# Kernel optimization log

Measured on AMD Instinct MI355X. Metric: run time of the kernel, lower is better.

The kernel has to match this reference:

```python
import jax, jax.numpy as jnp
import numpy as np

H = 8          # heads
D = 64         # head_dimension
EMB = 512      # embedding_dimension
B, S, XL, KK = 4, 1024, 1024, 32


def setup_inputs() -> dict:
    key = jax.random.key(0)
    ks = jax.random.split(key, 14)
    HD = H * D
    wsc = EMB ** -0.5
    return {
        "x": jax.random.normal(ks[0], (B, S, EMB), jnp.float32),
        "rel_pos": jax.random.normal(ks[1], (H, S, XL + S), jnp.float32) * 0.02,
        "xl_memory": jax.random.normal(ks[2], (B, XL, 2, HD), jnp.float32),
        "knn_retrieved": jax.random.normal(ks[3], (B, S, KK, 2, HD), jnp.float32),
        "Wq": jax.random.normal(ks[4], (HD, EMB), jnp.float32) * wsc,
        "bq": jnp.zeros((HD,), jnp.float32),
        "Wk": jax.random.normal(ks[5], (HD, EMB), jnp.float32) * wsc,
        "bk": jnp.zeros((HD,), jnp.float32),
        "Wv": jax.random.normal(ks[6], (HD, EMB), jnp.float32) * wsc,
        "bv": jnp.zeros((HD,), jnp.float32),
        "Wo": jax.random.normal(ks[7], (EMB, HD), jnp.float32) * (HD ** -0.5),
        "bo": jnp.zeros((EMB,), jnp.float32),
        "gate": jax.random.normal(ks[8], (H, 1, 1), jnp.float32),
    }


def _split_heads(t):
    # [b, s, h*d] -> [b, h, s, d]
    b, s, _ = t.shape
    return t.reshape(b, s, H, D).transpose(0, 2, 1, 3)


def reference(x, rel_pos, xl_memory, knn_retrieved,
              Wq, bq, Wk, bk, Wv, bv, Wo, bo, gate):
    scale = D ** -0.5
    b, s, _ = x.shape
    xl_len = xl_memory.shape[1]

    q = _split_heads(x @ Wq.T + bq)   # [b,h,s,d]
    k = _split_heads(x @ Wk.T + bk)
    v = _split_heads(x @ Wv.T + bv)

    # XL memory concat (keys/values stacked along dim -2 of xl_memory)
    k_mem = _split_heads(xl_memory[..., 0, :])
    v_mem = _split_heads(xl_memory[..., 1, :])
    k = jnp.concatenate((k_mem, k), axis=2)  # [b,h,j,d], j = xl+s
    v = jnp.concatenate((v_mem, v), axis=2)

    # local causal XL attention; note: rel_pos added BEFORE scaling (as in source)
    qk = jnp.einsum('bhid,bhjd->bhij', q, k)
    i, j = qk.shape[-2:]
    qk = (qk + rel_pos[..., -i:, -j:]) * scale
    mask = jnp.triu(jnp.ones((i, j), dtype=bool), j - i + 1)
    attn = jax.nn.softmax(jnp.where(mask, -jnp.inf, qk), axis=-1)
    qkv = jnp.einsum('bhij,bhjd->bhid', attn, v)

    # kNN external-memory attention over retrieved kv pairs
    kk = knn_retrieved.shape[2]
    k_ext = knn_retrieved[..., 0, :].reshape(b, s, kk, H, D).transpose(0, 3, 1, 2, 4)  # [b,h,s,k,d]
    v_ext = knn_retrieved[..., 1, :].reshape(b, s, kk, H, D).transpose(0, 3, 1, 2, 4)
    qk_ext = jnp.einsum('bhsd,bhskd->bhsk', q, k_ext) * scale
    attn_ext = jax.nn.softmax(qk_ext, axis=-1)
    qkv_ext = jnp.einsum('bhsk,bhskd->bhsd', attn_ext, v_ext)

    g = jax.nn.sigmoid(gate)                # [h,1,1] broadcasts over [b,h,s,d]
    merged = qkv * g + qkv_ext * (1.0 - g)

    out = merged.transpose(0, 2, 1, 3).reshape(b, s, H * D) @ Wo.T + bo

    # current kv memory: flatten heads, stack (k,v), drop the xl prefix
    key_flat = k.transpose(0, 2, 1, 3).reshape(b, j, H * D)
    val_flat = v.transpose(0, 2, 1, 3).reshape(b, j, H * D)
    current_kv_memory = jnp.stack((key_flat, val_flat), axis=-2)[:, xl_len:]

    return out, current_kv_memory
```

## Files before the change

kernel.cpp:

```cpp
#include <hip/hip_runtime.h>
#include <stdint.h>

#define H_ 8
#define D_ 64
#define EMBD 512
#define HD_ 512
#define B_ 4
#define S_ 1024
#define XL_ 1024
#define J_ 2048
#define KK_ 32
#define OUT1 (B_*S_*EMBD)

typedef __bf16 bf16x8 __attribute__((ext_vector_type(8)));
typedef float f32x4 __attribute__((ext_vector_type(4)));

__device__ __forceinline__ uint32_t pack2bf(float a, float b) {
    uint32_t ua = __builtin_bit_cast(uint32_t, a);
    uint32_t ub = __builtin_bit_cast(uint32_t, b);
    ua = (ua + 0x7FFFu + ((ua >> 16) & 1u)) >> 16;
    ub = (ub + 0x7FFFu + ((ub >> 16) & 1u)) >> 16;
    return ua | (ub << 16);
}

#define GPAD 72

__device__ __forceinline__ void gemm_tile_body(
    const float* __restrict__ A, const float* __restrict__ W,
    const float* __restrict__ bias, float* __restrict__ out, int mode,
    uint16_t* a_l, uint16_t* w_l, int m0, int n0)
{
    const int t    = threadIdx.x;
    const int wv   = t >> 6;
    const int lane = t & 63;
    const int quad = lane >> 4;
    const int l16  = lane & 15;
    const int lrow = t >> 2;
    const int lseg = (t & 3) * 16;

    const float* gab = A + (size_t)(m0 + lrow) * EMBD + lseg;
    const float* gwb = W + (size_t)(n0 + lrow) * EMBD + lseg;

    f32x4 zero = {0.f, 0.f, 0.f, 0.f};
    f32x4 acc[4] = {zero, zero, zero, zero};

    float4 a0 = *(const float4*)(gab);
    float4 a1 = *(const float4*)(gab + 4);
    float4 a2 = *(const float4*)(gab + 8);
    float4 a3 = *(const float4*)(gab + 12);
    float4 w0 = *(const float4*)(gwb);
    float4 w1 = *(const float4*)(gwb + 4);
    float4 w2 = *(const float4*)(gwb + 8);
    float4 w3 = *(const float4*)(gwb + 12);

    for (int k0 = 0; k0 < EMBD; k0 += 64) {
        uint32_t* pa = (uint32_t*)(a_l + lrow * GPAD + lseg);
        uint32_t* pw = (uint32_t*)(w_l + lrow * GPAD + lseg);
        pa[0] = pack2bf(a0.x, a0.y); pa[1] = pack2bf(a0.z, a0.w);
        pa[2] = pack2bf(a1.x, a1.y); pa[3] = pack2bf(a1.z, a1.w);
        pa[4] = pack2bf(a2.x, a2.y); pa[5] = pack2bf(a2.z, a2.w);
        pa[6] = pack2bf(a3.x, a3.y); pa[7] = pack2bf(a3.z, a3.w);
        pw[0] = pack2bf(w0.x, w0.y); pw[1] = pack2bf(w0.z, w0.w);
        pw[2] = pack2bf(w1.x, w1.y); pw[3] = pack2bf(w1.z, w1.w);
        pw[4] = pack2bf(w2.x, w2.y); pw[5] = pack2bf(w2.z, w2.w);
        pw[6] = pack2bf(w3.x, w3.y); pw[7] = pack2bf(w3.z, w3.w);
        __syncthreads();

        if (k0 + 64 < EMBD) {
            const float* ga = gab + k0 + 64;
            const float* gw = gwb + k0 + 64;
            a0 = *(const float4*)(ga);
            a1 = *(const float4*)(ga + 4);
            a2 = *(const float4*)(ga + 8);
            a3 = *(const float4*)(ga + 12);
            w0 = *(const float4*)(gw);
            w1 = *(const float4*)(gw + 4);
            w2 = *(const float4*)(gw + 8);
            w3 = *(const float4*)(gw + 12);
        }

        #pragma unroll
        for (int ks = 0; ks < 64; ks += 32) {
            bf16x8 af = *(const bf16x8*)(a_l + (wv*16 + l16) * GPAD + ks + quad*8);
            #pragma unroll
            for (int nt = 0; nt < 4; nt++) {
                bf16x8 wf = *(const bf16x8*)(w_l + (nt*16 + l16) * GPAD + ks + quad*8);
                acc[nt] = __builtin_amdgcn_mfma_f32_16x16x32_bf16(af, wf, acc[nt], 0, 0, 0);
            }
        }
        __syncthreads();
    }

    #pragma unroll
    for (int nt = 0; nt < 4; nt++) {
        const int col = n0 + nt*16 + l16;
        const float bvv = bias[col];
        #pragma unroll
        for (int r = 0; r < 4; r++) {
            const int row = m0 + wv*16 + quad*4 + r;
            const float v = acc[nt][r] + bvv;
            if (mode == 0)      out[(size_t)row * EMBD + col] = v;
            else if (mode == 1) out[(size_t)row * 1024 + col] = v;
            else                out[(size_t)row * 1024 + 512 + col] = v;
        }
    }
}

__global__ __launch_bounds__(256) void gemm_bt(
    const float* __restrict__ A, const float* __restrict__ W,
    const float* __restrict__ bias, float* __restrict__ out, int mode)
{
    __shared__ uint16_t a_l[64 * GPAD];
    __shared__ uint16_t w_l[64 * GPAD];
    gemm_tile_body(A, W, bias, out, mode, a_l, w_l, blockIdx.x * 64, blockIdx.y * 64);
}

__global__ __launch_bounds__(256) void gemm_qkv(
    const float* __restrict__ A,
    const float* __restrict__ Wq, const float* __restrict__ bq,
    const float* __restrict__ Wk, const float* __restrict__ bk,
    const float* __restrict__ Wv, const float* __restrict__ bv,
    float* __restrict__ q_ws, float* __restrict__ kv_out)
{
    __shared__ uint16_t a_l[64 * GPAD];
    __shared__ uint16_t w_l[64 * GPAD];
    const int mode = blockIdx.z;
    const float* W    = (mode == 0) ? Wq : (mode == 1) ? Wk : Wv;
    const float* bias = (mode == 0) ? bq : (mode == 1) ? bk : bv;
    float* out        = (mode == 0) ? q_ws : kv_out;
    gemm_tile_body(A, W, bias, out, mode, a_l, w_l, blockIdx.x * 64, blockIdx.y * 64);
}

#define APAD 72

__global__ __launch_bounds__(256) void attn_local(
    const float* __restrict__ q_ws,
    const float* __restrict__ xlm,
    const float* __restrict__ kv_cur,
    const float* __restrict__ rel,
    float* __restrict__ o_ws)
{
    __shared__ uint16_t qS[64][APAD];
    __shared__ uint16_t kS[64][APAD];
    __shared__ uint16_t vS[64][APAD];
    __shared__ uint16_t pS[4][16][APAD];

    const int t    = threadIdx.x;
    const int wv   = t >> 6;
    const int lane = t & 63;
    const int quad = lane >> 4;
    const int l16  = lane & 15;
    const int b    = blockIdx.z;
    const int h    = blockIdx.y;
    const int i0   = blockIdx.x * 64;

    const int irow0  = i0 + wv*16 + quad*4;
    const int ntiles = ((i0 + XL_ + 63) >> 6) + 1;
    const float scale = 0.125f;

    const int kj  = t >> 2;
    const int kdc = (t & 3) * 16;
    const int vj  = (t & 31) * 2;
    const int vdc = (t >> 5) * 8;

    {
        const int row = t >> 2;
        const int dc  = (t & 3) * 16;
        const float* g = q_ws + (size_t)(b*S_ + i0 + row) * HD_ + h*D_ + dc;
        float4 x0 = *(const float4*)(g);
        float4 x1 = *(const float4*)(g + 4);
        float4 x2 = *(const float4*)(g + 8);
        float4 x3 = *(const float4*)(g + 12);
        uint32_t* d = (uint32_t*)&qS[row][dc];
        d[0] = pack2bf(x0.x, x0.y); d[1] = pack2bf(x0.z, x0.w);
        d[2] = pack2bf(x1.x, x1.y); d[3] = pack2bf(x1.z, x1.w);
        d[4] = pack2bf(x2.x, x2.y); d[5] = pack2bf(x2.z, x2.w);
        d[6] = pack2bf(x3.x, x3.y); d[7] = pack2bf(x3.z, x3.w);
    }

    float4 kx0, kx1, kx2, kx3, va0, va1, vb0, vb1;
    {
        const int jg = kj;
        const float* g = (jg < XL_)
            ? xlm + ((size_t)(b*XL_ + jg) * 2) * HD_ + h*D_ + kdc
            : kv_cur + ((size_t)(b*S_ + (jg - XL_)) * 2) * HD_ + h*D_ + kdc;
        kx0 = *(const float4*)(g);
        kx1 = *(const float4*)(g + 4);
        kx2 = *(const float4*)(g + 8);
        kx3 = *(const float4*)(g + 12);
        const int jgv = vj;
        const float* g0 = (jgv < XL_)
            ? xlm + ((size_t)(b*XL_ + jgv) * 2 + 1) * HD_ + h*D_ + vdc
            : kv_cur + ((size_t)(b*S_ + (jgv - XL_)) * 2 + 1) * HD_ + h*D_ + vdc;
        va0 = *(const float4*)(g0);
        va1 = *(const float4*)(g0 + 4);
        vb0 = *(const float4*)(g0 + 2*HD_);
        vb1 = *(const float4*)(g0 + 2*HD_ + 4);
    }

    __syncthreads();
    const bf16x8 aq0 = *(const bf16x8*)&qS[wv*16 + l16][quad*8];
    const bf16x8 aq1 = *(const bf16x8*)&qS[wv*16 + l16][32 + quad*8];

    f32x4 zero = {0.f, 0.f, 0.f, 0.f};
    f32x4 accO[4] = {zero, zero, zero, zero};
    float m_r[4], l_r[4];
    #pragma unroll
    for (int r = 0; r < 4; r++) { m_r[r] = -1e30f; l_r[r] = 0.f; }

    const float* relbase = rel + ((size_t)h*S_ + irow0) * J_ + l16;

    for (int tix = 0; tix < ntiles; tix++) {
        const int j0 = tix << 6;
        {
            uint32_t* d = (uint32_t*)&kS[kj][kdc];
            d[0] = pack2bf(kx0.x, kx0.y); d[1] = pack2bf(kx0.z, kx0.w);
            d[2] = pack2bf(kx1.x, kx1.y); d[3] = pack2bf(kx1.z, kx1.w);
            d[4] = pack2bf(kx2.x, kx2.y); d[5] = pack2bf(kx2.z, kx2.w);
            d[6] = pack2bf(kx3.x, kx3.y); d[7] = pack2bf(kx3.z, kx3.w);
        }
        {
            *(uint32_t*)&vS[vdc+0][vj] = pack2bf(va0.x, vb0.x);
            *(uint32_t*)&vS[vdc+1][vj] = pack2bf(va0.y, vb0.y);
            *(uint32_t*)&vS[vdc+2][vj] = pack2bf(va0.z, vb0.z);
            *(uint32_t*)&vS[vdc+3][vj] = pack2bf(va0.w, vb0.w);
            *(uint32_t*)&vS[vdc+4][vj] = pack2bf(va1.x, vb1.x);
            *(uint32_t*)&vS[vdc+5][vj] = pack2bf(va1.y, vb1.y);
            *(uint32_t*)&vS[vdc+6][vj] = pack2bf(va1.z, vb1.z);
            *(uint32_t*)&vS[vdc+7][vj] = pack2bf(va1.w, vb1.w);
        }
        __syncthreads();

        if (tix + 1 < ntiles) {
            const int jg = j0 + 64 + kj;
            const float* g = (jg < XL_)
                ? xlm + ((size_t)(b*XL_ + jg) * 2) * HD_ + h*D_ + kdc
                : kv_cur + ((size_t)(b*S_ + (jg - XL_)) * 2) * HD_ + h*D_ + kdc;
            kx0 = *(const float4*)(g);
            kx1 = *(const float4*)(g + 4);
            kx2 = *(const float4*)(g + 8);
            kx3 = *(const float4*)(g + 12);
            const int jgv = j0 + 64 + vj;
            const float* g0 = (jgv < XL_)
                ? xlm + ((size_t)(b*XL_ + jgv) * 2 + 1) * HD_ + h*D_ + vdc
                : kv_cur + ((size_t)(b*S_ + (jgv - XL_)) * 2 + 1) * HD_ + h*D_ + vdc;
            va0 = *(const float4*)(g0);
            va1 = *(const float4*)(g0 + 4);
            vb0 = *(const float4*)(g0 + 2*HD_);
            vb1 = *(const float4*)(g0 + 2*HD_ + 4);
        }

        float srel[4][4];
        const float* rb = relbase + j0;
        #pragma unroll
        for (int r = 0; r < 4; r++)
            #pragma unroll
            for (int jt = 0; jt < 4; jt++)
                srel[r][jt] = rb[(size_t)r * J_ + jt*16];

        f32x4 sac[4] = {zero, zero, zero, zero};
        #pragma unroll
        for (int jt = 0; jt < 4; jt++) {
            bf16x8 bk0 = *(const bf16x8*)&kS[jt*16 + l16][quad*8];
            bf16x8 bk1 = *(const bf16x8*)&kS[jt*16 + l16][32 + quad*8];
            sac[jt] = __builtin_amdgcn_mfma_f32_16x16x32_bf16(aq0, bk0, sac[jt], 0, 0, 0);
            sac[jt] = __builtin_amdgcn_mfma_f32_16x16x32_bf16(aq1, bk1, sac[jt], 0, 0, 0);
        }

        const bool need_mask = (j0 + 64 > i0 + XL_);

        float p_[4][4];
        float alpha[4];
        #pragma unroll
        for (int r = 0; r < 4; r++) {
            const int irow = irow0 + r;
            float sv[4];
            #pragma unroll
            for (int jt = 0; jt < 4; jt++) {
                float s = (sac[jt][r] + srel[r][jt]) * scale;
                if (need_mask && (j0 + jt*16 + l16 > irow + XL_)) s = -1e30f;
                sv[jt] = s;
            }
            float mx = fmaxf(fmaxf(sv[0], sv[1]), fmaxf(sv[2], sv[3]));
            #pragma unroll
            for (int off = 8; off >= 1; off >>= 1)
                mx = fmaxf(mx, __shfl_xor(mx, off));
            const float mnew = fmaxf(m_r[r], mx);
            alpha[r] = __expf(m_r[r] - mnew);
            m_r[r] = mnew;
            float ps = 0.f;
            #pragma unroll
            for (int jt = 0; jt < 4; jt++) {
                p_[jt][r] = __expf(sv[jt] - mnew);
                ps += p_[jt][r];
            }
            #pragma unroll
            for (int off = 8; off >= 1; off >>= 1)
                ps += __shfl_xor(ps, off);
            l_r[r] = l_r[r] * alpha[r] + ps;
        }
        #pragma unroll
        for (int dt = 0; dt < 4; dt++)
            #pragma unroll
            for (int r = 0; r < 4; r++)
                accO[dt][r] *= alpha[r];

        #pragma unroll
        for (int jt = 0; jt < 4; jt++)
            #pragma unroll
            for (int r = 0; r < 4; r++)
                pS[wv][quad*4 + r][jt*16 + l16] = (uint16_t)pack2bf(p_[jt][r], 0.f);

        #pragma unroll
        for (int kc = 0; kc < 2; kc++) {
            bf16x8 ap = *(const bf16x8*)&pS[wv][l16][kc*32 + quad*8];
            #pragma unroll
            for (int dt = 0; dt < 4; dt++) {
                bf16x8 bv = *(const bf16x8*)&vS[dt*16 + l16][kc*32 + quad*8];
                accO[dt] = __builtin_amdgcn_mfma_f32_16x16x32_bf16(ap, bv, accO[dt], 0, 0, 0);
            }
        }
        __syncthreads();
    }

    #pragma unroll
    for (int r = 0; r < 4; r++) {
        const float inv = 1.f / l_r[r];
        float* o = o_ws + (size_t)(b*S_ + irow0 + r) * HD_ + h*D_ + l16;
        #pragma unroll
        for (int dt = 0; dt < 4; dt++)
            o[dt*16] = accO[dt][r] * inv;
    }
}

__global__ __launch_bounds__(512) void knn_merge(
    const float* __restrict__ q_ws, const float* __restrict__ knn,
    const float* __restrict__ o_ws, const float* __restrict__ gate,
    float* __restrict__ merged)
{
    __shared__ float p_s[H_][KK_];
    const int t    = threadIdx.x;
    const int wv   = t >> 6;
    const int lane = t & 63;
    const size_t bs = blockIdx.x;
    const float* base = knn + bs * (size_t)(KK_ * 2 * HD_);
    const float qv = q_ws[bs * HD_ + t];

    #pragma unroll 4
    for (int kk = 0; kk < KK_; kk++) {
        float pr = qv * base[(size_t)(kk*2) * HD_ + t];
        #pragma unroll
        for (int off = 32; off >= 1; off >>= 1)
            pr += __shfl_xor(pr, off);
        if (lane == 0) p_s[wv][kk] = pr;
    }
    __syncthreads();

    const float sval = p_s[wv][lane & 31] * 0.125f;
    float mx = sval;
    #pragma unroll
    for (int off = 16; off >= 1; off >>= 1)
        mx = fmaxf(mx, __shfl_xor(mx, off));
    const float e = __expf(sval - mx);
    float es = e;
    #pragma unroll
    for (int off = 16; off >= 1; off >>= 1)
        es += __shfl_xor(es, off);
    if (lane < 32) p_s[wv][lane] = e / es;
    __syncthreads();

    float acc = 0.f;
    #pragma unroll 4
    for (int kk = 0; kk < KK_; kk++)
        acc += p_s[wv][kk] * base[(size_t)(kk*2 + 1) * HD_ + t];

    const float g = 1.f / (1.f + __expf(-gate[wv]));
    const float o = o_ws[bs * HD_ + t];
    merged[bs * HD_ + t] = o * g + acc * (1.f - g);
}

extern "C" void kernel_launch(void* const* d_in, const int* in_sizes, int n_in,
                              void* d_out, int out_size, void* d_ws, size_t ws_size,
                              hipStream_t stream)
{
    (void)in_sizes; (void)n_in; (void)out_size; (void)ws_size;
    const float* x    = (const float*)d_in[0];
    const float* rel  = (const float*)d_in[1];
    const float* xlm  = (const float*)d_in[2];
    const float* knn  = (const float*)d_in[3];
    const float* Wq   = (const float*)d_in[4];
    const float* bq   = (const float*)d_in[5];
    const float* Wk   = (const float*)d_in[6];
    const float* bk   = (const float*)d_in[7];
    const float* Wv   = (const float*)d_in[8];
    const float* bv   = (const float*)d_in[9];
    const float* Wo   = (const float*)d_in[10];
    const float* bo   = (const float*)d_in[11];
    const float* gate = (const float*)d_in[12];

    float* out    = (float*)d_out;
    float* kv_out = out + OUT1;
    float* q_ws   = (float*)d_ws;
    float* o_ws   = q_ws + OUT1;
    float* mg_ws  = o_ws + OUT1;

    gemm_qkv<<<dim3(64, 8, 3), 256, 0, stream>>>(x, Wq, bq, Wk, bk, Wv, bv, q_ws, kv_out);
    attn_local<<<dim3(16, 8, 4), 256, 0, stream>>>(q_ws, xlm, kv_out, rel, o_ws);
    knn_merge<<<dim3(4096), 512, 0, stream>>>(q_ws, knn, o_ws, gate, mg_ws);
    gemm_bt<<<dim3(64, 8, 1), 256, 0, stream>>>(mg_ws, Wo, bo, out, 0);
}
```

Measured before the change: 934.6 us.

## Co-schedule kNN attention with local attention; fold gate merge into output GEMM

Local attention and kNN retrieval attention now run in one launch. Blocks 0-511 do the local attention tiles and blocks 512+ each handle one (b,s) kNN row using 256 threads covering two heads apiece. This lets the memory-bound kNN work (reading the large retrieved KV tensor) overlap with the compute-bound attention blocks. The gated merge of local and kNN outputs moves into the output projection's A-tile load, removing one kernel and one intermediate write and read. The risks are uneven block scheduling and extra register or shared-memory pressure in the combined kernel.

```diff
diff --git a/kernel.cpp b/kernel.cpp
--- a/kernel.cpp
+++ b/kernel.cpp
@@ -104,15 +104,6 @@
             else                out[(size_t)row * 1024 + 512 + col] = v;
         }
     }
-}
-
-__global__ __launch_bounds__(256) void gemm_bt(
-    const float* __restrict__ A, const float* __restrict__ W,
-    const float* __restrict__ bias, float* __restrict__ out, int mode)
-{
-    __shared__ uint16_t a_l[64 * GPAD];
-    __shared__ uint16_t w_l[64 * GPAD];
-    gemm_tile_body(A, W, bias, out, mode, a_l, w_l, blockIdx.x * 64, blockIdx.y * 64);
 }
 
 __global__ __launch_bounds__(256) void gemm_qkv(
@@ -131,28 +122,175 @@
     gemm_tile_body(A, W, bias, out, mode, a_l, w_l, blockIdx.x * 64, blockIdx.y * 64);
 }
 
+__global__ __launch_bounds__(256) void gemm_out(
+    const float* __restrict__ o_ws, const float* __restrict__ ext_ws,
+    const float* __restrict__ gate, const float* __restrict__ W,
+    const float* __restrict__ bias, float* __restrict__ out)
+{
+    __shared__ uint16_t a_l[64 * GPAD];
+    __shared__ uint16_t w_l[64 * GPAD];
+    const int t    = threadIdx.x;
+    const int m0   = blockIdx.x * 64;
+    const int n0   = blockIdx.y * 64;
+    const int wv   = t >> 6;
+    const int lane = t & 63;
+    const int quad = lane >> 4;
+    const int l16  = lane & 15;
+    const int lrow = t >> 2;
+    const int lseg = (t & 3) * 16;
+
+    const size_t arow = (size_t)(m0 + lrow) * HD_ + lseg;
+    const float* gob = o_ws + arow;
+    const float* geb = ext_ws + arow;
+    const float* gwb = W + (size_t)(n0 + lrow) * EMBD + lseg;
+
+    f32x4 zero = {0.f, 0.f, 0.f, 0.f};
+    f32x4 acc[4] = {zero, zero, zero, zero};
+
+    float4 o0 = *(const float4*)(gob);
+    float4 o1 = *(const float4*)(gob + 4);
+    float4 o2 = *(const float4*)(gob + 8);
+    float4 o3 = *(const float4*)(gob + 12);
+    float4 e0 = *(const float4*)(geb);
+    float4 e1 = *(const float4*)(geb + 4);
+    float4 e2 = *(const float4*)(geb + 8);
+    float4 e3 = *(const float4*)(geb + 12);
+    float4 w0 = *(const float4*)(gwb);
+    float4 w1 = *(const float4*)(gwb + 4);
+    float4 w2 = *(const float4*)(gwb + 8);
+    float4 w3 = *(const float4*)(gwb + 12);
+
+    for (int k0 = 0; k0 < EMBD; k0 += 64) {
+        const float gh = 1.f / (1.f + __expf(-gate[k0 >> 6]));
+        uint32_t* pa = (uint32_t*)(a_l + lrow * GPAD + lseg);
+        uint32_t* pw = (uint32_t*)(w_l + lrow * GPAD + lseg);
+        pa[0] = pack2bf(e0.x + (o0.x - e0.x)*gh, e0.y + (o0.y - e0.y)*gh);
+        pa[1] = pack2bf(e0.z + (o0.z - e0.z)*gh, e0.w + (o0.w - e0.w)*gh);
+        pa[2] = pack2bf(e1.x + (o1.x - e1.x)*gh, e1.y + (o1.y - e1.y)*gh);
+        pa[3] = pack2bf(e1.z + (o1.z - e1.z)*gh, e1.w + (o1.w - e1.w)*gh);
+        pa[4] = pack2bf(e2.x + (o2.x - e2.x)*gh, e2.y + (o2.y - e2.y)*gh);
+        pa[5] = pack2bf(e2.z + (o2.z - e2.z)*gh, e2.w + (o2.w - e2.w)*gh);
+        pa[6] = pack2bf(e3.x + (o3.x - e3.x)*gh, e3.y + (o3.y - e3.y)*gh);
+        pa[7] = pack2bf(e3.z + (o3.z - e3.z)*gh, e3.w + (o3.w - e3.w)*gh);
+        pw[0] = pack2bf(w0.x, w0.y); pw[1] = pack2bf(w0.z, w0.w);
+        pw[2] = pack2bf(w1.x, w1.y); pw[3] = pack2bf(w1.z, w1.w);
+        pw[4] = pack2bf(w2.x, w2.y); pw[5] = pack2bf(w2.z, w2.w);
+        pw[6] = pack2bf(w3.x, w3.y); pw[7] = pack2bf(w3.z, w3.w);
+        __syncthreads();
+
+        if (k0 + 64 < EMBD) {
+            const float* go = gob + k0 + 64;
+            const float* ge = geb + k0 + 64;
+            const float* gw = gwb + k0 + 64;
+            o0 = *(const float4*)(go);      o1 = *(const float4*)(go + 4);
+            o2 = *(const float4*)(go + 8);  o3 = *(const float4*)(go + 12);
+            e0 = *(const float4*)(ge);      e1 = *(const float4*)(ge + 4);
+            e2 = *(const float4*)(ge + 8);  e3 = *(const float4*)(ge + 12);
+            w0 = *(const float4*)(gw);      w1 = *(const float4*)(gw + 4);
+            w2 = *(const float4*)(gw + 8);  w3 = *(const float4*)(gw + 12);
+        }
+
+        #pragma unroll
+        for (int ks = 0; ks < 64; ks += 32) {
+            bf16x8 af = *(const bf16x8*)(a_l + (wv*16 + l16) * GPAD + ks + quad*8);
+            #pragma unroll
+            for (int nt = 0; nt < 4; nt++) {
+                bf16x8 wf = *(const bf16x8*)(w_l + (nt*16 + l16) * GPAD + ks + quad*8);
+                acc[nt] = __builtin_amdgcn_mfma_f32_16x16x32_bf16(af, wf, acc[nt], 0, 0, 0);
+            }
+        }
+        __syncthreads();
+    }
+
+    #pragma unroll
+    for (int nt = 0; nt < 4; nt++) {
+        const int col = n0 + nt*16 + l16;
+        const float bvv = bias[col];
+        #pragma unroll
+        for (int r = 0; r < 4; r++) {
+            const int row = m0 + wv*16 + quad*4 + r;
+            out[(size_t)row * EMBD + col] = acc[nt][r] + bvv;
+        }
+    }
+}
+
 #define APAD 72
 
-__global__ __launch_bounds__(256) void attn_local(
+__global__ __launch_bounds__(256) void attn_knn(
     const float* __restrict__ q_ws,
     const float* __restrict__ xlm,
     const float* __restrict__ kv_cur,
     const float* __restrict__ rel,
-    float* __restrict__ o_ws)
+    const float* __restrict__ knn,
+    float* __restrict__ o_ws,
+    float* __restrict__ ext_ws)
 {
-    __shared__ uint16_t qS[64][APAD];
-    __shared__ uint16_t kS[64][APAD];
-    __shared__ uint16_t vS[64][APAD];
-    __shared__ uint16_t pS[4][16][APAD];
-
+    __shared__ __align__(16) uint8_t smem[36864];
+    const int bid  = blockIdx.x;
     const int t    = threadIdx.x;
     const int wv   = t >> 6;
     const int lane = t & 63;
+
+    if (bid >= 512) {
+        float* p_s = (float*)smem;
+        const size_t bs = bid - 512;
+        const float* base = knn + bs * (size_t)(KK_ * 2 * HD_);
+        const int h0 = wv;
+        const int h1 = wv + 4;
+        const float qv0 = q_ws[bs * HD_ + h0*64 + lane];
+        const float qv1 = q_ws[bs * HD_ + h1*64 + lane];
+
+        #pragma unroll 4
+        for (int kk = 0; kk < KK_; kk++) {
+            const float* krow = base + (size_t)(kk*2) * HD_;
+            float pr0 = qv0 * krow[h0*64 + lane];
+            float pr1 = qv1 * krow[h1*64 + lane];
+            #pragma unroll
+            for (int off = 32; off >= 1; off >>= 1) {
+                pr0 += __shfl_xor(pr0, off);
+                pr1 += __shfl_xor(pr1, off);
+            }
+            if (lane == 0) { p_s[h0*KK_ + kk] = pr0; p_s[h1*KK_ + kk] = pr1; }
+        }
+        __syncthreads();
+
+        const int hh = wv + 4 * (lane >> 5);
+        const int kidx = lane & 31;
+        const float sval = p_s[hh*KK_ + kidx] * 0.125f;
+        float mx = sval;
+        #pragma unroll
+        for (int off = 16; off >= 1; off >>= 1)
+            mx = fmaxf(mx, __shfl_xor(mx, off));
+        const float e = __expf(sval - mx);
+        float es = e;
+        #pragma unroll
+        for (int off = 16; off >= 1; off >>= 1)
+            es += __shfl_xor(es, off);
+        p_s[hh*KK_ + kidx] = e / es;
+        __syncthreads();
+
+        float acc0 = 0.f, acc1 = 0.f;
+        #pragma unroll 4
+        for (int kk = 0; kk < KK_; kk++) {
+            const float* vrow = base + (size_t)(kk*2 + 1) * HD_;
+            acc0 += p_s[h0*KK_ + kk] * vrow[h0*64 + lane];
+            acc1 += p_s[h1*KK_ + kk] * vrow[h1*64 + lane];
+        }
+        ext_ws[bs * HD_ + h0*64 + lane] = acc0;
+        ext_ws[bs * HD_ + h1*64 + lane] = acc1;
+        return;
+    }
+
+    uint16_t (*qS)[APAD]     = (uint16_t(*)[APAD])(smem);
+    uint16_t (*kS)[APAD]     = (uint16_t(*)[APAD])(smem + 9216);
+    uint16_t (*vS)[APAD]     = (uint16_t(*)[APAD])(smem + 18432);
+    uint16_t (*pS)[16][APAD] = (uint16_t(*)[16][APAD])(smem + 27648);
+
     const int quad = lane >> 4;
     const int l16  = lane & 15;
-    const int b    = blockIdx.z;
-    const int h    = blockIdx.y;
-    const int i0   = blockIdx.x * 64;
+    const int b    = bid >> 7;
+    const int h    = (bid >> 4) & 7;
+    const int i0   = (bid & 15) * 64;
 
     const int irow0  = i0 + wv*16 + quad*4;
     const int ntiles = ((i0 + XL_ + 63) >> 6) + 1;
@@ -333,52 +471,6 @@
     }
 }
 
-__global__ __launch_bounds__(512) void knn_merge(
-    const float* __restrict__ q_ws, const float* __restrict__ knn,
-    const float* __restrict__ o_ws, const float* __restrict__ gate,
-    float* __restrict__ merged)
-{
-    __shared__ float p_s[H_][KK_];
-    const int t    = threadIdx.x;
-    const int wv   = t >> 6;
-    const int lane = t & 63;
-    const size_t bs = blockIdx.x;
-    const float* base = knn + bs * (size_t)(KK_ * 2 * HD_);
-    const float qv = q_ws[bs * HD_ + t];
-
-    #pragma unroll 4
-    for (int kk = 0; kk < KK_; kk++) {
-        float pr = qv * base[(size_t)(kk*2) * HD_ + t];
-        #pragma unroll
-        for (int off = 32; off >= 1; off >>= 1)
-            pr += __shfl_xor(pr, off);
-        if (lane == 0) p_s[wv][kk] = pr;
-    }
-    __syncthreads();
-
-    const float sval = p_s[wv][lane & 31] * 0.125f;
-    float mx = sval;
-    #pragma unroll
-    for (int off = 16; off >= 1; off >>= 1)
-        mx = fmaxf(mx, __shfl_xor(mx, off));
-    const float e = __expf(sval - mx);
-    float es = e;
-    #pragma unroll
-    for (int off = 16; off >= 1; off >>= 1)
-        es += __shfl_xor(es, off);
-    if (lane < 32) p_s[wv][lane] = e / es;
-    __syncthreads();
-
-    float acc = 0.f;
-    #pragma unroll 4
-    for (int kk = 0; kk < KK_; kk++)
-        acc += p_s[wv][kk] * base[(size_t)(kk*2 + 1) * HD_ + t];
-
-    const float g = 1.f / (1.f + __expf(-gate[wv]));
-    const float o = o_ws[bs * HD_ + t];
-    merged[bs * HD_ + t] = o * g + acc * (1.f - g);
-}
-
 extern "C" void kernel_launch(void* const* d_in, const int* in_sizes, int n_in,
                               void* d_out, int out_size, void* d_ws, size_t ws_size,
                               hipStream_t stream)
@@ -402,10 +494,9 @@
     float* kv_out = out + OUT1;
     float* q_ws   = (float*)d_ws;
     float* o_ws   = q_ws + OUT1;
-    float* mg_ws  = o_ws + OUT1;
+    float* ext_ws = o_ws + OUT1;
 
     gemm_qkv<<<dim3(64, 8, 3), 256, 0, stream>>>(x, Wq, bq, Wk, bk, Wv, bv, q_ws, kv_out);
-    attn_local<<<dim3(16, 8, 4), 256, 0, stream>>>(q_ws, xlm, kv_out, rel, o_ws);
-    knn_merge<<<dim3(4096), 512, 0, stream>>>(q_ws, knn, o_ws, gate, mg_ws);
-    gemm_bt<<<dim3(64, 8, 1), 256, 0, stream>>>(mg_ws, Wo, bo, out, 0);
+    attn_knn<<<dim3(4608), 256, 0, stream>>>(q_ws, xlm, kv_out, rel, knn, o_ws, ext_ws);
+    gemm_out<<<dim3(64, 8), 256, 0, stream>>>(o_ws, ext_ws, gate, Wo, bo, out);
 }
```

After: 913.4 us. 1.02x faster.
